# Kernel tuning notes

Measured on AMD Instinct MI355X. Metric: run time of the kernel, lower is better.

The kernel has to match this reference:

```python
import jax, jax.numpy as jnp
from jax import lax
import numpy as np

# ---- init hyperparameters (from init_kwargs) ----
STRIDE = 1
DP_CHANNELS = 1
ATOM_R = 8
ATOM_C = 8
NUMB_ATOM = 128
T_SC = 3
K = 256
BATCH = 32
IMG = 64


def setup_inputs() -> dict:
    key = jax.random.key(0)
    k1, k2 = jax.random.split(key)
    Y = jax.random.normal(k1, (BATCH, DP_CHANNELS, IMG, IMG), dtype=jnp.float32)
    # ConvTranspose2d weight layout: (numb_atom, dp_channels, atom_c, atom_r)
    W = jax.random.normal(k2, (NUMB_ATOM, DP_CHANNELS, ATOM_C, ATOM_R), dtype=jnp.float32)
    # normalise_weights(): each (i, j) filter divided by its L2 norm
    W = W / jnp.sqrt(jnp.sum(W ** 2, axis=(2, 3), keepdims=True))
    return {"Y": Y, "W_D": W}


def _conv_D(X, W):
    # PyTorch ConvTranspose2d (stride=1, no padding): full convolution with
    # spatially-flipped kernel; W is (in=numb_atom, out=dp_channels, kh, kw).
    kh, kw = W.shape[2], W.shape[3]
    return lax.conv_general_dilated(
        X, jnp.flip(W, (2, 3)), (1, 1),
        [(kh - 1, kh - 1), (kw - 1, kw - 1)],
        dimension_numbers=('NCHW', 'IOHW', 'NCHW'))


def _conv_Dt(R, Wt):
    # PyTorch Conv2d (VALID, stride=1): Wt is (out=numb_atom, in=dp, kh, kw)
    return lax.conv_general_dilated(
        R, Wt, (1, 1), 'VALID', dimension_numbers=('NCHW', 'OIHW', 'NCHW'))


def _hard_threshold_k(X, k):
    # keep the k largest-|.| entries per sample (over flattened C,H,W)
    B = X.shape[0]
    flat = X.reshape(B, -1)
    _, idx = lax.top_k(jnp.abs(flat), k)                      # [B, k]
    vals = jnp.take_along_axis(flat, idx, axis=1)             # [B, k]
    out = jnp.zeros_like(flat).at[jnp.arange(B)[:, None], idx].set(vals)
    return out.reshape(X.shape)


def _linesearch(Y, X, W, Wt, k):
    R = Y - _conv_D(X, W)
    g = _conv_Dt(R, Wt)
    l2_start = jnp.sum(R ** 2)

    def attempt(alpha):
        Xu = _hard_threshold_k(X + alpha * g, k)
        err = jnp.sum((Y - _conv_D(Xu, W)) ** 2)
        return Xu, err

    Xu0, err0 = attempt(jnp.float32(1.0))

    def cond(s):
        _, _, err, count = s
        return (err >= l2_start) & (count <= 15)

    def body(s):
        alpha, _, _, count = s
        alpha = alpha * jnp.float32(0.5)
        Xu, err = attempt(alpha)
        return (alpha, Xu, err, count + 1)

    alpha, Xu, err, _ = lax.while_loop(
        cond, body, (jnp.float32(1.0), Xu0, err0, jnp.int32(0)))
    return Xu, err, alpha


def reference(Y, W_D):
    # D_trans.weight = D.weight.permute(0,1,3,2) -> (numb_atom, dp, atom_r, atom_c)
    Wt = jnp.swapaxes(W_D, 2, 3)
    kh, kw = Wt.shape[2], Wt.shape[3]
    B, _, H, W_sp = Y.shape
    X = jnp.zeros((B, W_D.shape[0], H - kh + 1, W_sp - kw + 1), dtype=Y.dtype)
    for _ in range(T_SC):
        X, _, _ = _linesearch(Y, X, W_D, Wt, K)
    return X
```

## Files before the change

### kernel.cpp

```cpp
#include <hip/hip_runtime.h>
#include <stdint.h>

#define NB   32
#define NCH  128
#define IMG  64
#define IMG2 4096
#define OH   57
#define OHW  3249
#define CHW  415872
#define KTOP 256
#define NATT 17
#define NS   32
#define SCAP 512
#define NCAP 1536
#define NBUCK 8192
#define HSHIFT 18
#define TGT  512
#define RSTRIDE 72
#define NZB  257
#define BMW  12996

typedef unsigned long long ull;

__global__ void k_init(int* support_cnt) {
    if (threadIdx.x < NB) support_cnt[threadIdx.x] = 0;
}

__global__ __launch_bounds__(256) void k_resid(
    const float* __restrict__ Y, const float* __restrict__ W,
    const int* __restrict__ support_cnt, const uint32_t* __restrict__ support_idx,
    const float* __restrict__ support_val, float* __restrict__ Rg, double* __restrict__ l2part,
    uint32_t* __restrict__ hist, int* __restrict__ cand_cnt)
{
    int bx = blockIdx.x, tid = threadIdx.x;
    if (bx >= NB) {
        int zb = bx - NB;
        if (zb < 256) {
            ((uint4*)hist)[zb * 256 + tid] = make_uint4(0u, 0u, 0u, 0u);
        } else {
            ((uint4*)cand_cnt)[tid] = make_uint4(0u, 0u, 0u, 0u);
        }
        return;
    }
    int b = bx;
    __shared__ float Rs[IMG2];
    const float4* Y4 = (const float4*)(Y + b * IMG2);
    float4* R4 = (float4*)Rs;
    for (int i = tid; i < IMG2 / 4; i += 256) R4[i] = Y4[i];
    __syncthreads();
    int n = support_cnt[b];
    for (int task = tid; task < n * 64; task += 256) {
        int i = task >> 6, tap = task & 63, p = tap >> 3, q = tap & 7;
        uint32_t idx = support_idx[b * KTOP + i];
        float val = support_val[b * KTOP + i];
        int c = idx / OHW, rem = idx % OHW, s = rem / OH, t = rem % OH;
        float w = W[c * 64 + p * 8 + q];
        atomicAdd(&Rs[(s + p) * IMG + (t + q)], -val * w);
    }
    __syncthreads();
    double acc = 0.0;
    for (int i = tid; i < IMG2; i += 256) {
        float v = Rs[i];
        Rg[b * IMG2 + i] = v;
        acc += (double)v * (double)v;
    }
    __shared__ double red[256];
    red[tid] = acc; __syncthreads();
    for (int s2 = 128; s2 > 0; s2 >>= 1) { if (tid < s2) red[tid] += red[tid + s2]; __syncthreads(); }
    if (tid == 0) l2part[b] = red[0];
}

__global__ __launch_bounds__(256) void k_conv(
    const float* __restrict__ Rg, const float* __restrict__ W,
    float* __restrict__ g_out, uint32_t* __restrict__ hist)
{
    int b = blockIdx.x, cg0 = blockIdx.y, tid = threadIdx.x;
    __shared__ float Rs[71 * 72];
    __shared__ uint32_t hl[NBUCK];
    for (int i = tid; i < 71 * 72; i += 256) Rs[i] = 0.f;
    for (int i = tid; i < NBUCK; i += 256) hl[i] = 0u;
    __syncthreads();
    const float4* R4 = (const float4*)(Rg + b * IMG2);
    for (int i = tid; i < 1024; i += 256) {
        int row = i >> 4, col4 = (i & 15) * 4;
        *(float4*)&Rs[row * 72 + col4] = R4[i];
    }
    __syncthreads();
    int csub = tid >> 7;
    int tile = tid & 127;
    bool active = tile < 120;
    int tr = active ? tile / 15 : 0;
    int tc = active ? tile % 15 : 0;
    int s0 = tr * 8, t0 = tc * 4;

    for (int sub = 0; sub < 4; ++sub) {
        int c = cg0 * 8 + sub * 2 + csub;
        int c_s = __builtin_amdgcn_readfirstlane(c);
        const float* Wc = W + c_s * 64;

        float acc[8][4];
#pragma unroll
        for (int r = 0; r < 8; ++r)
#pragma unroll
            for (int cc = 0; cc < 4; ++cc) acc[r][cc] = 0.f;

#pragma unroll
        for (int rho = 0; rho < 15; ++rho) {
            float rb[12];
            const float* rp = &Rs[(s0 + rho) * 72 + t0];
            *(float4*)&rb[0] = *(const float4*)rp;
            *(float4*)&rb[4] = *(const float4*)(rp + 4);
            *(float4*)&rb[8] = *(const float4*)(rp + 8);
#pragma unroll
            for (int r = 0; r < 8; ++r) {
                const int p = rho - r;
                if (p >= 0 && p < 8) {
#pragma unroll
                    for (int q = 0; q < 8; ++q) {
                        float wv = Wc[q * 8 + p];
#pragma unroll
                        for (int cc = 0; cc < 4; ++cc)
                            acc[r][cc] = fmaf(rb[cc + q], wv, acc[r][cc]);
                    }
                }
            }
        }
        if (active) {
            float* go = g_out + (size_t)(b * NCH + c) * OHW;
#pragma unroll
            for (int r = 0; r < 8; ++r) {
                int s = s0 + r;
                if (s < OH) {
#pragma unroll
                    for (int cc = 0; cc < 4; ++cc) {
                        int t = t0 + cc;
                        if (t < OH) {
                            float v = acc[r][cc];
                            go[s * OH + t] = v;
                            uint32_t bits = __float_as_uint(v) & 0x7fffffffu;
                            atomicAdd(&hl[bits >> HSHIFT], 1u);
                        }
                    }
                }
            }
        }
    }
    __syncthreads();
    for (int i = tid; i < NBUCK; i += 256) {
        uint32_t v = hl[i];
        if (v) atomicAdd(&hist[b * NBUCK + i], v);
    }
}

__global__ __launch_bounds__(256) void k_thresh(const uint32_t* __restrict__ hist,
                                                uint32_t* __restrict__ thr) {
    int b = blockIdx.x, tid = threadIdx.x;
    uint32_t h[32];
    uint32_t s = 0;
    const uint32_t* hb = hist + b * NBUCK + tid * 32;
#pragma unroll
    for (int k = 0; k < 32; ++k) { h[k] = hb[k]; s += h[k]; }
    __shared__ uint32_t buf[2][256];
    int cur = 0;
    buf[0][tid] = s;
    __syncthreads();
    for (int d = 1; d < 256; d <<= 1) {
        uint32_t v = buf[cur][tid];
        if (tid + d < 256) v += buf[cur][tid + d];
        buf[cur ^ 1][tid] = v;
        cur ^= 1;
        __syncthreads();
    }
    uint32_t sufme = buf[cur][tid];
    uint32_t base  = (tid < 255) ? buf[cur][tid + 1] : 0u;
    if (tid == 0 && buf[cur][0] < TGT) thr[b] = 0u;
    if (base < TGT && sufme >= TGT) {
        uint32_t acc = base; int bk = 0;
#pragma unroll
        for (int k = 31; k >= 0; --k) {
            acc += h[k];
            if (acc >= TGT) { bk = tid * 32 + k; break; }
        }
        thr[b] = (uint32_t)bk << HSHIFT;
    }
}

__global__ __launch_bounds__(256) void k_collect(
    const float* __restrict__ g, const uint32_t* __restrict__ thr,
    int* __restrict__ cand_cnt, uint32_t* __restrict__ cand_idx, float* __restrict__ cand_g)
{
    int b = blockIdx.y;
    int i4 = blockIdx.x * 256 + threadIdx.x;
    if (i4 >= CHW / 4) return;
    int slice = blockIdx.x & (NS - 1);
    uint32_t tb = thr[b];
    float4 v4 = ((const float4*)(g + (size_t)b * CHW))[i4];
    float vv[4] = { v4.x, v4.y, v4.z, v4.w };
#pragma unroll
    for (int k = 0; k < 4; ++k) {
        uint32_t bits = __float_as_uint(vv[k]) & 0x7fffffffu;
        if (bits >= tb) {
            int pos = atomicAdd(&cand_cnt[b * NS + slice], 1);
            if (pos < SCAP) {
                cand_idx[(b * NS + slice) * SCAP + pos] = (uint32_t)(i4 * 4 + k);
                cand_g[(b * NS + slice) * SCAP + pos] = vv[k];
            }
        }
    }
}

__global__ __launch_bounds__(1024) void k_suppg(
    const float* __restrict__ g,
    const int* __restrict__ support_cnt, const uint32_t* __restrict__ support_idx,
    const int* __restrict__ cand_cnt, const uint32_t* __restrict__ cand_idx,
    const float* __restrict__ cand_g,
    uint32_t* __restrict__ ns_idx, float* __restrict__ ns_g, uint32_t* __restrict__ ns_pk,
    float* __restrict__ sup_g, uint32_t* __restrict__ sup_pk)
{
    int b = blockIdx.x, tid = threadIdx.x, lane = tid & 63;
    __shared__ uint32_t bm[BMW];
    __shared__ int cnts[NS];
    __shared__ ull ck[NCAP];
    __shared__ float cg_l[NCAP];
    __shared__ int nns_sh;
    int n = support_cnt[b];
    for (int i = tid; i < BMW / 4; i += 1024) ((uint4*)bm)[i] = make_uint4(0u, 0u, 0u, 0u);
    if (tid < NS) cnts[tid] = min(cand_cnt[b * NS + tid], SCAP);
    if (tid == 0) nns_sh = 0;
    __syncthreads();
    if (tid < KTOP) {
        if (tid < n) {
            uint32_t idx = support_idx[b * KTOP + tid];
            atomicOr(&bm[idx >> 5], 1u << (idx & 31));
            float gv = g[(size_t)b * CHW + idx];
            sup_g[b * KTOP + tid] = gv;
            int c = idx / OHW, r = idx % OHW, s = r / OH, t = r % OH;
            sup_pk[b * KTOP + tid] = (uint32_t)((c << 12) | (s << 6) | t);
        } else {
            sup_g[b * KTOP + tid] = 0.f;
            sup_pk[b * KTOP + tid] = 0u;
        }
    }
    __syncthreads();
    for (int t0 = tid; t0 < NS * SCAP; t0 += 1024) {
        int s = t0 >> 9, j = t0 & (SCAP - 1);
        bool keep = false; uint32_t idx = 0; float gv = 0.f;
        if (j < cnts[s]) {
            idx = cand_idx[(b * NS + s) * SCAP + j];
            gv = cand_g[(b * NS + s) * SCAP + j];
            keep = ((bm[idx >> 5] >> (idx & 31)) & 1u) == 0u;
        }
        ull mk = __ballot(keep);
        if (mk) {
            int basep = 0;
            if (lane == 0) basep = atomicAdd(&nns_sh, (int)__popcll(mk));
            basep = __shfl(basep, 0, 64);
            if (keep) {
                int p = basep + (int)__popcll(mk & ((1ull << lane) - 1ull));
                if (p < NCAP) {
                    ck[p] = ((ull)(__float_as_uint(gv) & 0x7fffffffu) << 32) | (ull)(uint32_t)(~idx);
                    cg_l[p] = gv;
                }
            }
        }
    }
    __syncthreads();
    int nns = min(nns_sh, NCAP);
    int nns8 = (nns + 7) & ~7;
    for (int i = nns + tid; i < nns8; i += 1024) ck[i] = 0ull;
    __syncthreads();
    ull myk[2]; int myr[2];
#pragma unroll
    for (int q = 0; q < 2; ++q) { int i = tid + 1024 * q; myk[q] = (i < nns) ? ck[i] : 0ull; myr[q] = 0; }
    for (int j = 0; j < nns8; j += 8) {
        ull t0 = ck[j], t1 = ck[j+1], t2 = ck[j+2], t3 = ck[j+3];
        ull t4 = ck[j+4], t5 = ck[j+5], t6 = ck[j+6], t7 = ck[j+7];
#pragma unroll
        for (int q = 0; q < 2; ++q) {
            myr[q] += ((t0 > myk[q]) ? 1 : 0) + ((t1 > myk[q]) ? 1 : 0)
                    + ((t2 > myk[q]) ? 1 : 0) + ((t3 > myk[q]) ? 1 : 0)
                    + ((t4 > myk[q]) ? 1 : 0) + ((t5 > myk[q]) ? 1 : 0)
                    + ((t6 > myk[q]) ? 1 : 0) + ((t7 > myk[q]) ? 1 : 0);
        }
    }
#pragma unroll
    for (int q = 0; q < 2; ++q) {
        int i = tid + 1024 * q;
        if (i < nns && myr[q] < KTOP) {
            uint32_t idx = ~(uint32_t)myk[q];
            int r = myr[q];
            ns_idx[b * KTOP + r] = idx;
            ns_g[b * KTOP + r] = cg_l[i];
            int c = idx / OHW, rr = idx % OHW, s = rr / OH, t = rr % OH;
            ns_pk[b * KTOP + r] = (uint32_t)((c << 12) | (s << 6) | t);
        }
    }
}

__global__ __launch_bounds__(1024) void k_att2(
    const float* __restrict__ Y, const float* __restrict__ W,
    const int* __restrict__ support_cnt, const uint32_t* __restrict__ support_idx,
    const float* __restrict__ support_val,
    const float* __restrict__ sup_g, const uint32_t* __restrict__ sup_pk,
    const uint32_t* __restrict__ ns_idx, const float* __restrict__ ns_g,
    const uint32_t* __restrict__ ns_pk,
    uint32_t* __restrict__ sel_idx, float* __restrict__ sel_val, double* __restrict__ err)
{
    int a = blockIdx.x, b = blockIdx.y, tid = threadIdx.x;
    int lane = tid & 63, wid = tid >> 6;
    float alpha = ldexpf(1.f, -a);
    int n = support_cnt[b];

    __shared__ float Wlds[NCH * 64];
    __shared__ float recon[64 * RSTRIDE];
    __shared__ ull kA[KTOP];
    __shared__ ull kB[KTOP];
    __shared__ float s_v[KTOP];
    __shared__ uint32_t s_pk2[KTOP];
    __shared__ double redd[16];

    uint32_t nsi = 0, pk_ns = 0, spi = 0, pk_sup = 0;
    float v_ns = 0.f, v_sup = 0.f;
    ull k_ns = 0, k_sup = 0;
    if (wid < 4) {
        nsi = ns_idx[b * KTOP + tid];
        v_ns = alpha * ns_g[b * KTOP + tid];
        pk_ns = ns_pk[b * KTOP + tid];
        k_ns = ((ull)(__float_as_uint(v_ns) & 0x7fffffffu) << 32) | (ull)(uint32_t)(~nsi);
        kA[tid] = k_ns;
        if (tid < n) {
            spi = support_idx[b * KTOP + tid];
            v_sup = fmaf(alpha, sup_g[b * KTOP + tid], support_val[b * KTOP + tid]);
            pk_sup = sup_pk[b * KTOP + tid];
        } else {
            spi = (uint32_t)(CHW + tid);
            v_sup = 0.f; pk_sup = 0u;
        }
        k_sup = ((ull)(__float_as_uint(v_sup) & 0x7fffffffu) << 32) | (ull)(uint32_t)(~spi);
        kB[tid] = k_sup;
    }
    __syncthreads();

    if (wid < 4) {
        int cb_ns = 0, cb_sup = 0;
        for (int j = 0; j < KTOP; j += 8) {
            ull t0 = kB[j], t1 = kB[j+1], t2 = kB[j+2], t3 = kB[j+3];
            ull t4 = kB[j+4], t5 = kB[j+5], t6 = kB[j+6], t7 = kB[j+7];
            cb_ns  += ((t0 > k_ns) ? 1 : 0) + ((t1 > k_ns) ? 1 : 0)
                    + ((t2 > k_ns) ? 1 : 0) + ((t3 > k_ns) ? 1 : 0)
                    + ((t4 > k_ns) ? 1 : 0) + ((t5 > k_ns) ? 1 : 0)
                    + ((t6 > k_ns) ? 1 : 0) + ((t7 > k_ns) ? 1 : 0);
            cb_sup += ((t0 > k_sup) ? 1 : 0) + ((t1 > k_sup) ? 1 : 0)
                    + ((t2 > k_sup) ? 1 : 0) + ((t3 > k_sup) ? 1 : 0)
                    + ((t4 > k_sup) ? 1 : 0) + ((t5 > k_sup) ? 1 : 0)
                    + ((t6 > k_sup) ? 1 : 0) + ((t7 > k_sup) ? 1 : 0);
        }
        int rank_ns = tid + cb_ns;
        int lo = 0, hi = KTOP;
        while (lo < hi) { int mid = (lo + hi) >> 1; if (kA[mid] > k_sup) lo = mid + 1; else hi = mid; }
        int rank_sup = lo + cb_sup;
        size_t o = ((size_t)a * NB + b) * KTOP;
        if (rank_ns < KTOP) {
            s_v[rank_ns] = v_ns; s_pk2[rank_ns] = pk_ns;
            sel_idx[o + rank_ns] = nsi; sel_val[o + rank_ns] = v_ns;
        }
        if (rank_sup < KTOP) {
            s_v[rank_sup] = v_sup; s_pk2[rank_sup] = pk_sup;
            sel_idx[o + rank_sup] = spi; sel_val[o + rank_sup] = v_sup;
        }
    } else {
        for (int i = tid - 256; i < 64 * RSTRIDE; i += 768) recon[i] = 0.f;
        for (int i = tid - 256; i < (NCH * 64) / 4; i += 768)
            ((float4*)Wlds)[i] = ((const float4*)W)[i];
    }
    __syncthreads();

    for (int task = tid; task < KTOP * 64; task += 1024) {
        int i = task >> 6, tap = task & 63, p = tap >> 3, q = tap & 7;
        uint32_t pk = s_pk2[i];
        float val = s_v[i];
        int c = pk >> 12, s = (pk >> 6) & 63, t = pk & 63;
        atomicAdd(&recon[(s + p) * RSTRIDE + (t + q)], val * Wlds[c * 64 + tap]);
    }
    __syncthreads();

    float4 y4 = ((const float4*)(Y + b * IMG2))[tid];
    int row = tid >> 4, col = (tid & 15) * 4;
    const float* rr = &recon[row * RSTRIDE + col];
    double accd = 0.0;
    float d0 = y4.x - rr[0]; accd += (double)d0 * (double)d0;
    float d1 = y4.y - rr[1]; accd += (double)d1 * (double)d1;
    float d2 = y4.z - rr[2]; accd += (double)d2 * (double)d2;
    float d3 = y4.w - rr[3]; accd += (double)d3 * (double)d3;
    for (int d = 32; d > 0; d >>= 1) accd += __shfl_xor(accd, d, 64);
    if (lane == 0) redd[wid] = accd;
    __syncthreads();
    if (tid == 0) {
        double e = 0.0;
#pragma unroll
        for (int w2 = 0; w2 < 16; ++w2) e += redd[w2];
        err[a * NB + b] = e;
    }
}

__global__ __launch_bounds__(256) void k_update(
    const double* __restrict__ l2part, const double* __restrict__ err,
    const uint32_t* __restrict__ sel_idx, const float* __restrict__ sel_val,
    int* __restrict__ support_cnt, uint32_t* __restrict__ support_idx, float* __restrict__ support_val)
{
    int b = blockIdx.x, tid = threadIdx.x;
    __shared__ double esum[NATT + 1];
    __shared__ int sel_sh;
    if (tid < NATT) {
        double e = 0.0;
        for (int b2 = 0; b2 < NB; ++b2) e += err[tid * NB + b2];
        esum[tid] = e;
    } else if (tid == NATT) {
        double l2 = 0.0;
        for (int b2 = 0; b2 < NB; ++b2) l2 += l2part[b2];
        esum[NATT] = l2;
    }
    __syncthreads();
    if (tid == 0) {
        double l2 = esum[NATT];
        int sel = NATT - 1;
        for (int a2 = 0; a2 < NATT; ++a2) if (esum[a2] < l2) { sel = a2; break; }
        sel_sh = sel;
    }
    __syncthreads();
    int a = sel_sh;
    __shared__ uint32_t ki[KTOP];
    __shared__ float kv[KTOP];
    ki[tid] = sel_idx[((size_t)a * NB + b) * KTOP + tid];
    kv[tid] = sel_val[((size_t)a * NB + b) * KTOP + tid];
    __syncthreads();
    uint32_t me = ki[tid];
    int rank = 0;
    for (int j = 0; j < KTOP; j += 8) {
        uint32_t a0 = ki[j], a1 = ki[j+1], a2 = ki[j+2], a3 = ki[j+3];
        uint32_t a4 = ki[j+4], a5 = ki[j+5], a6 = ki[j+6], a7 = ki[j+7];
        rank += ((a0 < me) ? 1 : 0) + ((a1 < me) ? 1 : 0) + ((a2 < me) ? 1 : 0) + ((a3 < me) ? 1 : 0)
              + ((a4 < me) ? 1 : 0) + ((a5 < me) ? 1 : 0) + ((a6 < me) ? 1 : 0) + ((a7 < me) ? 1 : 0);
    }
    support_idx[b * KTOP + rank] = me;
    support_val[b * KTOP + rank] = kv[tid];
    if (tid == 0) support_cnt[b] = KTOP;
}

__global__ void k_outzero(float4* __restrict__ out) {
    int i = blockIdx.x * 256 + threadIdx.x;
    if (i < (NB * CHW) / 4) out[i] = make_float4(0.f, 0.f, 0.f, 0.f);
}

__global__ void k_scatter(const uint32_t* __restrict__ support_idx, const float* __restrict__ support_val,
                          float* __restrict__ out) {
    int b = blockIdx.x, tid = threadIdx.x;
    if (tid < KTOP) out[(size_t)b * CHW + support_idx[b * KTOP + tid]] = support_val[b * KTOP + tid];
}

static size_t align256(size_t x) { return (x + 255) & ~(size_t)255; }

extern "C" void kernel_launch(void* const* d_in, const int* in_sizes, int n_in,
                              void* d_out, int out_size, void* d_ws, size_t ws_size,
                              hipStream_t stream)
{
    const float* Y = (const float*)d_in[0];
    const float* W = (const float*)d_in[1];
    float* out = (float*)d_out;

    char* p = (char*)d_ws;
    size_t off = 0;
    auto carve = [&](size_t bytes) { void* r = p + off; off = align256(off + bytes); return r; };
    float*    Rg          = (float*)   carve(NB * IMG2 * sizeof(float));
    uint32_t* hist        = (uint32_t*)carve((size_t)NB * NBUCK * sizeof(uint32_t));
    uint32_t* thr         = (uint32_t*)carve(NB * sizeof(uint32_t));
    int*      cand_cnt    = (int*)     carve(NB * NS * sizeof(int));
    double*   l2part      = (double*)  carve(NB * sizeof(double));
    double*   err         = (double*)  carve(NATT * NB * sizeof(double));
    int*      support_cnt = (int*)     carve(NB * sizeof(int));
    uint32_t* support_idx = (uint32_t*)carve(NB * KTOP * sizeof(uint32_t));
    float*    support_val = (float*)   carve(NB * KTOP * sizeof(float));
    uint32_t* sel_idx     = (uint32_t*)carve((size_t)NATT * NB * KTOP * sizeof(uint32_t));
    float*    sel_val     = (float*)   carve((size_t)NATT * NB * KTOP * sizeof(float));
    uint32_t* cand_idx    = (uint32_t*)carve((size_t)NB * NS * SCAP * sizeof(uint32_t));
    float*    cand_g      = (float*)   carve((size_t)NB * NS * SCAP * sizeof(float));
    uint32_t* ns_idx      = (uint32_t*)carve(NB * KTOP * sizeof(uint32_t));
    float*    ns_gbuf     = (float*)   carve(NB * KTOP * sizeof(float));
    uint32_t* ns_pk       = (uint32_t*)carve(NB * KTOP * sizeof(uint32_t));
    float*    sup_gbuf    = (float*)   carve(NB * KTOP * sizeof(float));
    uint32_t* sup_pk      = (uint32_t*)carve(NB * KTOP * sizeof(uint32_t));
    (void)ws_size; (void)in_sizes; (void)n_in; (void)out_size;

    k_init<<<1, 64, 0, stream>>>(support_cnt);
    for (int t = 0; t < 3; ++t) {
        k_resid<<<NB + NZB, 256, 0, stream>>>(Y, W, support_cnt, support_idx, support_val,
                                              Rg, l2part, hist, cand_cnt);
        k_conv<<<dim3(NB, 16), 256, 0, stream>>>(Rg, W, out, hist);
        k_thresh<<<NB, 256, 0, stream>>>(hist, thr);
        k_collect<<<dim3((CHW / 4 + 255) / 256, NB), 256, 0, stream>>>(out, thr, cand_cnt, cand_idx, cand_g);
        k_suppg<<<NB, 1024, 0, stream>>>(out, support_cnt, support_idx,
                                         cand_cnt, cand_idx, cand_g,
                                         ns_idx, ns_gbuf, ns_pk, sup_gbuf, sup_pk);
        k_att2<<<dim3(NATT, NB), 1024, 0, stream>>>(Y, W, support_cnt, support_idx, support_val,
                                                    sup_gbuf, sup_pk, ns_idx, ns_gbuf, ns_pk,
                                                    sel_idx, sel_val, err);
        k_update<<<NB, 256, 0, stream>>>(l2part, err, sel_idx, sel_val,
                                         support_cnt, support_idx, support_val);
    }
    k_outzero<<<((NB * CHW) / 4 + 255) / 256, 256, 0, stream>>>((float4*)out);
    k_scatter<<<NB, 256, 0, stream>>>(support_idx, support_val, out);
}
```

Baseline: 671.0 us.

## Fuse candidate selection and all line-search attempts into one per-sample kernel

Merges the support/candidate ranking kernel and the per-alpha attempt kernel into one 1024-thread block per sample. That block loops serially over all 17 step sizes, keeping Y, W and the candidate lists in shared memory. The support update is folded into the start of the residual kernel, and the final scatter reads the selected attempt directly. Together this removes the init, update and scatter launches and several global round-trips. The cost is parallelism: the attempt grid shrinks from 17×32 blocks to 32 blocks, so the 17 attempts now run one after another on few compute units.

```diff
diff --git a/kernel.cpp b/kernel.cpp
--- a/kernel.cpp
+++ b/kernel.cpp
@@ -22,14 +22,12 @@
 
 typedef unsigned long long ull;
 
-__global__ void k_init(int* support_cnt) {
-    if (threadIdx.x < NB) support_cnt[threadIdx.x] = 0;
-}
-
 __global__ __launch_bounds__(256) void k_resid(
     const float* __restrict__ Y, const float* __restrict__ W,
-    const int* __restrict__ support_cnt, const uint32_t* __restrict__ support_idx,
-    const float* __restrict__ support_val, float* __restrict__ Rg, double* __restrict__ l2part,
+    int do_update, const double* __restrict__ l2_prev, const double* __restrict__ errv,
+    const uint32_t* __restrict__ sel_idx, const float* __restrict__ sel_val,
+    uint32_t* __restrict__ support_idx, float* __restrict__ support_val,
+    float* __restrict__ Rg, double* __restrict__ l2_out,
     uint32_t* __restrict__ hist, int* __restrict__ cand_cnt)
 {
     int bx = blockIdx.x, tid = threadIdx.x;
@@ -43,16 +41,49 @@
         return;
     }
     int b = bx;
+    __shared__ uint32_t sidx_l[KTOP];
+    __shared__ float sval_l[KTOP];
+    __shared__ double esum[NATT + 1];
+    __shared__ int sel_sh;
+    int n = 0;
+    if (do_update) {
+        if (tid < NATT) {
+            double e = 0.0;
+            for (int b2 = 0; b2 < NB; ++b2) e += errv[tid * NB + b2];
+            esum[tid] = e;
+        } else if (tid == NATT) {
+            double l2 = 0.0;
+            for (int b2 = 0; b2 < NB; ++b2) l2 += l2_prev[b2];
+            esum[NATT] = l2;
+        }
+        __syncthreads();
+        if (tid == 0) {
+            double l2 = esum[NATT];
+            int sel = NATT - 1;
+            for (int a2 = 0; a2 < NATT; ++a2) if (esum[a2] < l2) { sel = a2; break; }
+            sel_sh = sel;
+        }
+        __syncthreads();
+        int a = sel_sh;
+        size_t o = ((size_t)a * NB + b) * KTOP + tid;
+        uint32_t ii = sel_idx[o];
+        float vv = sel_val[o];
+        sidx_l[tid] = ii; sval_l[tid] = vv;
+        support_idx[b * KTOP + tid] = ii;
+        support_val[b * KTOP + tid] = vv;
+        n = KTOP;
+    }
+    __syncthreads();
+
     __shared__ float Rs[IMG2];
     const float4* Y4 = (const float4*)(Y + b * IMG2);
     float4* R4 = (float4*)Rs;
     for (int i = tid; i < IMG2 / 4; i += 256) R4[i] = Y4[i];
     __syncthreads();
-    int n = support_cnt[b];
     for (int task = tid; task < n * 64; task += 256) {
         int i = task >> 6, tap = task & 63, p = tap >> 3, q = tap & 7;
-        uint32_t idx = support_idx[b * KTOP + i];
-        float val = support_val[b * KTOP + i];
+        uint32_t idx = sidx_l[i];
+        float val = sval_l[i];
         int c = idx / OHW, rem = idx % OHW, s = rem / OH, t = rem % OH;
         float w = W[c * 64 + p * 8 + q];
         atomicAdd(&Rs[(s + p) * IMG + (t + q)], -val * w);
@@ -67,7 +98,7 @@
     __shared__ double red[256];
     red[tid] = acc; __syncthreads();
     for (int s2 = 128; s2 > 0; s2 >>= 1) { if (tid < s2) red[tid] += red[tid + s2]; __syncthreads(); }
-    if (tid == 0) l2part[b] = red[0];
+    if (tid == 0) l2_out[b] = red[0];
 }
 
 __global__ __launch_bounds__(256) void k_conv(
@@ -209,36 +240,45 @@
     }
 }
 
-__global__ __launch_bounds__(1024) void k_suppg(
-    const float* __restrict__ g,
-    const int* __restrict__ support_cnt, const uint32_t* __restrict__ support_idx,
+__global__ __launch_bounds__(1024) void k_fat(
+    const float* __restrict__ g, const float* __restrict__ Y, const float* __restrict__ W,
+    int n_sup, const uint32_t* __restrict__ support_idx, const float* __restrict__ support_val,
     const int* __restrict__ cand_cnt, const uint32_t* __restrict__ cand_idx,
     const float* __restrict__ cand_g,
-    uint32_t* __restrict__ ns_idx, float* __restrict__ ns_g, uint32_t* __restrict__ ns_pk,
-    float* __restrict__ sup_g, uint32_t* __restrict__ sup_pk)
+    uint32_t* __restrict__ sel_idx, float* __restrict__ sel_val, double* __restrict__ err)
 {
-    int b = blockIdx.x, tid = threadIdx.x, lane = tid & 63;
-    __shared__ uint32_t bm[BMW];
-    __shared__ int cnts[NS];
+    int b = blockIdx.x, tid = threadIdx.x, lane = tid & 63, wid = tid >> 6;
+    __shared__ union UU {
+        uint32_t bm[BMW];
+        struct { float Y[IMG2]; float W[NCH * 64]; } yw;
+    } u;
     __shared__ ull ck[NCAP];
     __shared__ float cg_l[NCAP];
-    __shared__ int nns_sh;
-    int n = support_cnt[b];
-    for (int i = tid; i < BMW / 4; i += 1024) ((uint4*)bm)[i] = make_uint4(0u, 0u, 0u, 0u);
+    __shared__ float recon[64 * RSTRIDE];
+    __shared__ uint32_t A_idx[KTOP]; __shared__ float A_g[KTOP]; __shared__ uint32_t A_pk[KTOP];
+    __shared__ uint32_t B_idx[KTOP]; __shared__ float B_x[KTOP];
+    __shared__ float B_g[KTOP]; __shared__ uint32_t B_pk[KTOP];
+    __shared__ ull kA[KTOP]; __shared__ ull kB[KTOP];
+    __shared__ float s_v[KTOP]; __shared__ uint32_t s_pk2[KTOP];
+    __shared__ double redd[16];
+    __shared__ int cnts[NS]; __shared__ int nns_sh;
+
+    for (int i = tid; i < BMW / 4; i += 1024) ((uint4*)u.bm)[i] = make_uint4(0u, 0u, 0u, 0u);
     if (tid < NS) cnts[tid] = min(cand_cnt[b * NS + tid], SCAP);
     if (tid == 0) nns_sh = 0;
     __syncthreads();
     if (tid < KTOP) {
-        if (tid < n) {
+        if (tid < n_sup) {
             uint32_t idx = support_idx[b * KTOP + tid];
-            atomicOr(&bm[idx >> 5], 1u << (idx & 31));
-            float gv = g[(size_t)b * CHW + idx];
-            sup_g[b * KTOP + tid] = gv;
+            atomicOr(&u.bm[idx >> 5], 1u << (idx & 31));
+            B_idx[tid] = idx;
+            B_x[tid] = support_val[b * KTOP + tid];
+            B_g[tid] = g[(size_t)b * CHW + idx];
             int c = idx / OHW, r = idx % OHW, s = r / OH, t = r % OH;
-            sup_pk[b * KTOP + tid] = (uint32_t)((c << 12) | (s << 6) | t);
+            B_pk[tid] = (uint32_t)((c << 12) | (s << 6) | t);
         } else {
-            sup_g[b * KTOP + tid] = 0.f;
-            sup_pk[b * KTOP + tid] = 0u;
+            B_idx[tid] = (uint32_t)(CHW + tid);
+            B_x[tid] = 0.f; B_g[tid] = 0.f; B_pk[tid] = 0u;
         }
     }
     __syncthreads();
@@ -248,7 +288,7 @@
         if (j < cnts[s]) {
             idx = cand_idx[(b * NS + s) * SCAP + j];
             gv = cand_g[(b * NS + s) * SCAP + j];
-            keep = ((bm[idx >> 5] >> (idx & 31)) & 1u) == 0u;
+            keep = ((u.bm[idx >> 5] >> (idx & 31)) & 1u) == 0u;
         }
         ull mk = __ballot(keep);
         if (mk) {
@@ -256,10 +296,10 @@
             if (lane == 0) basep = atomicAdd(&nns_sh, (int)__popcll(mk));
             basep = __shfl(basep, 0, 64);
             if (keep) {
-                int p = basep + (int)__popcll(mk & ((1ull << lane) - 1ull));
-                if (p < NCAP) {
-                    ck[p] = ((ull)(__float_as_uint(gv) & 0x7fffffffu) << 32) | (ull)(uint32_t)(~idx);
-                    cg_l[p] = gv;
+                int p2 = basep + (int)__popcll(mk & ((1ull << lane) - 1ull));
+                if (p2 < NCAP) {
+                    ck[p2] = ((ull)(__float_as_uint(gv) & 0x7fffffffu) << 32) | (ull)(uint32_t)(~idx);
+                    cg_l[p2] = gv;
                 }
             }
         }
@@ -269,155 +309,144 @@
     int nns8 = (nns + 7) & ~7;
     for (int i = nns + tid; i < nns8; i += 1024) ck[i] = 0ull;
     __syncthreads();
-    ull myk[2]; int myr[2];
-#pragma unroll
-    for (int q = 0; q < 2; ++q) { int i = tid + 1024 * q; myk[q] = (i < nns) ? ck[i] : 0ull; myr[q] = 0; }
-    for (int j = 0; j < nns8; j += 8) {
-        ull t0 = ck[j], t1 = ck[j+1], t2 = ck[j+2], t3 = ck[j+3];
-        ull t4 = ck[j+4], t5 = ck[j+5], t6 = ck[j+6], t7 = ck[j+7];
+    {
+        ull myk[2]; int myr[2];
+#pragma unroll
+        for (int q = 0; q < 2; ++q) { int i = tid + 1024 * q; myk[q] = (i < nns) ? ck[i] : 0ull; myr[q] = 0; }
+        for (int j = 0; j < nns8; j += 8) {
+            ull t0 = ck[j], t1 = ck[j+1], t2 = ck[j+2], t3 = ck[j+3];
+            ull t4 = ck[j+4], t5 = ck[j+5], t6 = ck[j+6], t7 = ck[j+7];
+#pragma unroll
+            for (int q = 0; q < 2; ++q) {
+                myr[q] += ((t0 > myk[q]) ? 1 : 0) + ((t1 > myk[q]) ? 1 : 0)
+                        + ((t2 > myk[q]) ? 1 : 0) + ((t3 > myk[q]) ? 1 : 0)
+                        + ((t4 > myk[q]) ? 1 : 0) + ((t5 > myk[q]) ? 1 : 0)
+                        + ((t6 > myk[q]) ? 1 : 0) + ((t7 > myk[q]) ? 1 : 0);
+            }
+        }
 #pragma unroll
         for (int q = 0; q < 2; ++q) {
-            myr[q] += ((t0 > myk[q]) ? 1 : 0) + ((t1 > myk[q]) ? 1 : 0)
-                    + ((t2 > myk[q]) ? 1 : 0) + ((t3 > myk[q]) ? 1 : 0)
-                    + ((t4 > myk[q]) ? 1 : 0) + ((t5 > myk[q]) ? 1 : 0)
-                    + ((t6 > myk[q]) ? 1 : 0) + ((t7 > myk[q]) ? 1 : 0);
-        }
-    }
-#pragma unroll
-    for (int q = 0; q < 2; ++q) {
-        int i = tid + 1024 * q;
-        if (i < nns && myr[q] < KTOP) {
-            uint32_t idx = ~(uint32_t)myk[q];
-            int r = myr[q];
-            ns_idx[b * KTOP + r] = idx;
-            ns_g[b * KTOP + r] = cg_l[i];
-            int c = idx / OHW, rr = idx % OHW, s = rr / OH, t = rr % OH;
-            ns_pk[b * KTOP + r] = (uint32_t)((c << 12) | (s << 6) | t);
-        }
-    }
-}
-
-__global__ __launch_bounds__(1024) void k_att2(
-    const float* __restrict__ Y, const float* __restrict__ W,
-    const int* __restrict__ support_cnt, const uint32_t* __restrict__ support_idx,
-    const float* __restrict__ support_val,
-    const float* __restrict__ sup_g, const uint32_t* __restrict__ sup_pk,
-    const uint32_t* __restrict__ ns_idx, const float* __restrict__ ns_g,
-    const uint32_t* __restrict__ ns_pk,
-    uint32_t* __restrict__ sel_idx, float* __restrict__ sel_val, double* __restrict__ err)
-{
-    int a = blockIdx.x, b = blockIdx.y, tid = threadIdx.x;
-    int lane = tid & 63, wid = tid >> 6;
-    float alpha = ldexpf(1.f, -a);
-    int n = support_cnt[b];
-
-    __shared__ float Wlds[NCH * 64];
-    __shared__ float recon[64 * RSTRIDE];
-    __shared__ ull kA[KTOP];
-    __shared__ ull kB[KTOP];
-    __shared__ float s_v[KTOP];
-    __shared__ uint32_t s_pk2[KTOP];
-    __shared__ double redd[16];
-
-    uint32_t nsi = 0, pk_ns = 0, spi = 0, pk_sup = 0;
-    float v_ns = 0.f, v_sup = 0.f;
-    ull k_ns = 0, k_sup = 0;
-    if (wid < 4) {
-        nsi = ns_idx[b * KTOP + tid];
-        v_ns = alpha * ns_g[b * KTOP + tid];
-        pk_ns = ns_pk[b * KTOP + tid];
-        k_ns = ((ull)(__float_as_uint(v_ns) & 0x7fffffffu) << 32) | (ull)(uint32_t)(~nsi);
-        kA[tid] = k_ns;
-        if (tid < n) {
-            spi = support_idx[b * KTOP + tid];
-            v_sup = fmaf(alpha, sup_g[b * KTOP + tid], support_val[b * KTOP + tid]);
-            pk_sup = sup_pk[b * KTOP + tid];
+            int i = tid + 1024 * q;
+            if (i < nns && myr[q] < KTOP) {
+                uint32_t idx = ~(uint32_t)myk[q];
+                int r = myr[q];
+                A_idx[r] = idx;
+                A_g[r] = cg_l[i];
+                int c = idx / OHW, rr = idx % OHW, s = rr / OH, t = rr % OH;
+                A_pk[r] = (uint32_t)((c << 12) | (s << 6) | t);
+            }
+        }
+    }
+    for (int i = tid; i < IMG2 / 4; i += 1024)
+        ((float4*)u.yw.Y)[i] = ((const float4*)(Y + b * IMG2))[i];
+    for (int i = tid; i < (NCH * 64) / 4; i += 1024)
+        ((float4*)u.yw.W)[i] = ((const float4*)W)[i];
+    __syncthreads();
+
+    for (int a = 0; a < NATT; ++a) {
+        float alpha = ldexpf(1.f, -a);
+        float v_ns = 0.f, v_sup = 0.f;
+        ull k_ns = 0, k_sup = 0;
+        if (tid < KTOP) {
+            v_ns = alpha * A_g[tid];
+            k_ns = ((ull)(__float_as_uint(v_ns) & 0x7fffffffu) << 32) | (ull)(uint32_t)(~A_idx[tid]);
+            kA[tid] = k_ns;
+            v_sup = fmaf(alpha, B_g[tid], B_x[tid]);
+            k_sup = ((ull)(__float_as_uint(v_sup) & 0x7fffffffu) << 32) | (ull)(uint32_t)(~B_idx[tid]);
+            kB[tid] = k_sup;
         } else {
-            spi = (uint32_t)(CHW + tid);
-            v_sup = 0.f; pk_sup = 0u;
-        }
-        k_sup = ((ull)(__float_as_uint(v_sup) & 0x7fffffffu) << 32) | (ull)(uint32_t)(~spi);
-        kB[tid] = k_sup;
-    }
-    __syncthreads();
-
-    if (wid < 4) {
-        int cb_ns = 0, cb_sup = 0;
-        for (int j = 0; j < KTOP; j += 8) {
-            ull t0 = kB[j], t1 = kB[j+1], t2 = kB[j+2], t3 = kB[j+3];
-            ull t4 = kB[j+4], t5 = kB[j+5], t6 = kB[j+6], t7 = kB[j+7];
-            cb_ns  += ((t0 > k_ns) ? 1 : 0) + ((t1 > k_ns) ? 1 : 0)
-                    + ((t2 > k_ns) ? 1 : 0) + ((t3 > k_ns) ? 1 : 0)
-                    + ((t4 > k_ns) ? 1 : 0) + ((t5 > k_ns) ? 1 : 0)
-                    + ((t6 > k_ns) ? 1 : 0) + ((t7 > k_ns) ? 1 : 0);
-            cb_sup += ((t0 > k_sup) ? 1 : 0) + ((t1 > k_sup) ? 1 : 0)
-                    + ((t2 > k_sup) ? 1 : 0) + ((t3 > k_sup) ? 1 : 0)
-                    + ((t4 > k_sup) ? 1 : 0) + ((t5 > k_sup) ? 1 : 0)
-                    + ((t6 > k_sup) ? 1 : 0) + ((t7 > k_sup) ? 1 : 0);
-        }
-        int rank_ns = tid + cb_ns;
-        int lo = 0, hi = KTOP;
-        while (lo < hi) { int mid = (lo + hi) >> 1; if (kA[mid] > k_sup) lo = mid + 1; else hi = mid; }
-        int rank_sup = lo + cb_sup;
-        size_t o = ((size_t)a * NB + b) * KTOP;
-        if (rank_ns < KTOP) {
-            s_v[rank_ns] = v_ns; s_pk2[rank_ns] = pk_ns;
-            sel_idx[o + rank_ns] = nsi; sel_val[o + rank_ns] = v_ns;
-        }
-        if (rank_sup < KTOP) {
-            s_v[rank_sup] = v_sup; s_pk2[rank_sup] = pk_sup;
-            sel_idx[o + rank_sup] = spi; sel_val[o + rank_sup] = v_sup;
-        }
-    } else {
-        for (int i = tid - 256; i < 64 * RSTRIDE; i += 768) recon[i] = 0.f;
-        for (int i = tid - 256; i < (NCH * 64) / 4; i += 768)
-            ((float4*)Wlds)[i] = ((const float4*)W)[i];
-    }
-    __syncthreads();
-
-    for (int task = tid; task < KTOP * 64; task += 1024) {
-        int i = task >> 6, tap = task & 63, p = tap >> 3, q = tap & 7;
-        uint32_t pk = s_pk2[i];
-        float val = s_v[i];
-        int c = pk >> 12, s = (pk >> 6) & 63, t = pk & 63;
-        atomicAdd(&recon[(s + p) * RSTRIDE + (t + q)], val * Wlds[c * 64 + tap]);
-    }
-    __syncthreads();
-
-    float4 y4 = ((const float4*)(Y + b * IMG2))[tid];
-    int row = tid >> 4, col = (tid & 15) * 4;
-    const float* rr = &recon[row * RSTRIDE + col];
-    double accd = 0.0;
-    float d0 = y4.x - rr[0]; accd += (double)d0 * (double)d0;
-    float d1 = y4.y - rr[1]; accd += (double)d1 * (double)d1;
-    float d2 = y4.z - rr[2]; accd += (double)d2 * (double)d2;
-    float d3 = y4.w - rr[3]; accd += (double)d3 * (double)d3;
-    for (int d = 32; d > 0; d >>= 1) accd += __shfl_xor(accd, d, 64);
-    if (lane == 0) redd[wid] = accd;
-    __syncthreads();
-    if (tid == 0) {
-        double e = 0.0;
-#pragma unroll
-        for (int w2 = 0; w2 < 16; ++w2) e += redd[w2];
-        err[a * NB + b] = e;
-    }
-}
-
-__global__ __launch_bounds__(256) void k_update(
-    const double* __restrict__ l2part, const double* __restrict__ err,
+            for (int i = tid - 256; i < 64 * RSTRIDE; i += 768) recon[i] = 0.f;
+        }
+        __syncthreads();
+        if (tid < KTOP) {
+            int cb_ns = 0, cb_sup = 0;
+            for (int j = 0; j < KTOP; j += 8) {
+                ull t0 = kB[j], t1 = kB[j+1], t2 = kB[j+2], t3 = kB[j+3];
+                ull t4 = kB[j+4], t5 = kB[j+5], t6 = kB[j+6], t7 = kB[j+7];
+                cb_ns  += ((t0 > k_ns) ? 1 : 0) + ((t1 > k_ns) ? 1 : 0)
+                        + ((t2 > k_ns) ? 1 : 0) + ((t3 > k_ns) ? 1 : 0)
+                        + ((t4 > k_ns) ? 1 : 0) + ((t5 > k_ns) ? 1 : 0)
+                        + ((t6 > k_ns) ? 1 : 0) + ((t7 > k_ns) ? 1 : 0);
+                cb_sup += ((t0 > k_sup) ? 1 : 0) + ((t1 > k_sup) ? 1 : 0)
+                        + ((t2 > k_sup) ? 1 : 0) + ((t3 > k_sup) ? 1 : 0)
+                        + ((t4 > k_sup) ? 1 : 0) + ((t5 > k_sup) ? 1 : 0)
+                        + ((t6 > k_sup) ? 1 : 0) + ((t7 > k_sup) ? 1 : 0);
+            }
+            int rank_ns = tid + cb_ns;
+            int lo = 0, hi = KTOP;
+            while (lo < hi) { int mid = (lo + hi) >> 1; if (kA[mid] > k_sup) lo = mid + 1; else hi = mid; }
+            int rank_sup = lo + cb_sup;
+            size_t o = ((size_t)a * NB + b) * KTOP;
+            if (rank_ns < KTOP) {
+                s_v[rank_ns] = v_ns; s_pk2[rank_ns] = A_pk[tid];
+                sel_idx[o + rank_ns] = A_idx[tid]; sel_val[o + rank_ns] = v_ns;
+            }
+            if (rank_sup < KTOP) {
+                s_v[rank_sup] = v_sup; s_pk2[rank_sup] = B_pk[tid];
+                sel_idx[o + rank_sup] = B_idx[tid]; sel_val[o + rank_sup] = v_sup;
+            }
+        }
+        __syncthreads();
+        {
+            int tap = lane, p = tap >> 3, q = tap & 7;
+            uint32_t pks[16]; float vals[16];
+#pragma unroll
+            for (int it = 0; it < 16; ++it) {
+                int i = wid + it * 16;
+                pks[it] = s_pk2[i]; vals[it] = s_v[i];
+            }
+            float wv[16];
+#pragma unroll
+            for (int it = 0; it < 16; ++it) wv[it] = u.yw.W[(pks[it] >> 12) * 64 + tap];
+#pragma unroll
+            for (int it = 0; it < 16; ++it) {
+                uint32_t pk = pks[it];
+                int s = (pk >> 6) & 63, t = pk & 63;
+                atomicAdd(&recon[(s + p) * RSTRIDE + (t + q)], vals[it] * wv[it]);
+            }
+        }
+        __syncthreads();
+        float4 y4 = ((const float4*)u.yw.Y)[tid];
+        int row = tid >> 4, col = (tid & 15) * 4;
+        const float* rr = &recon[row * RSTRIDE + col];
+        double accd = 0.0;
+        float d0 = y4.x - rr[0]; accd += (double)d0 * (double)d0;
+        float d1 = y4.y - rr[1]; accd += (double)d1 * (double)d1;
+        float d2 = y4.z - rr[2]; accd += (double)d2 * (double)d2;
+        float d3 = y4.w - rr[3]; accd += (double)d3 * (double)d3;
+        for (int d = 32; d > 0; d >>= 1) accd += __shfl_xor(accd, d, 64);
+        if (lane == 0) redd[wid] = accd;
+        __syncthreads();
+        if (tid == 0) {
+            double e = 0.0;
+#pragma unroll
+            for (int w2 = 0; w2 < 16; ++w2) e += redd[w2];
+            err[a * NB + b] = e;
+        }
+        __syncthreads();
+    }
+}
+
+__global__ void k_outzero(float4* __restrict__ out) {
+    int i = blockIdx.x * 256 + threadIdx.x;
+    if (i < (NB * CHW) / 4) out[i] = make_float4(0.f, 0.f, 0.f, 0.f);
+}
+
+__global__ __launch_bounds__(256) void k_scafin(
+    const double* __restrict__ l2_prev, const double* __restrict__ errv,
     const uint32_t* __restrict__ sel_idx, const float* __restrict__ sel_val,
-    int* __restrict__ support_cnt, uint32_t* __restrict__ support_idx, float* __restrict__ support_val)
+    float* __restrict__ out)
 {
     int b = blockIdx.x, tid = threadIdx.x;
     __shared__ double esum[NATT + 1];
     __shared__ int sel_sh;
     if (tid < NATT) {
         double e = 0.0;
-        for (int b2 = 0; b2 < NB; ++b2) e += err[tid * NB + b2];
+        for (int b2 = 0; b2 < NB; ++b2) e += errv[tid * NB + b2];
         esum[tid] = e;
     } else if (tid == NATT) {
         double l2 = 0.0;
-        for (int b2 = 0; b2 < NB; ++b2) l2 += l2part[b2];
+        for (int b2 = 0; b2 < NB; ++b2) l2 += l2_prev[b2];
         esum[NATT] = l2;
     }
     __syncthreads();
@@ -429,33 +458,8 @@
     }
     __syncthreads();
     int a = sel_sh;
-    __shared__ uint32_t ki[KTOP];
-    __shared__ float kv[KTOP];
-    ki[tid] = sel_idx[((size_t)a * NB + b) * KTOP + tid];
-    kv[tid] = sel_val[((size_t)a * NB + b) * KTOP + tid];
-    __syncthreads();
-    uint32_t me = ki[tid];
-    int rank = 0;
-    for (int j = 0; j < KTOP; j += 8) {
-        uint32_t a0 = ki[j], a1 = ki[j+1], a2 = ki[j+2], a3 = ki[j+3];
-        uint32_t a4 = ki[j+4], a5 = ki[j+5], a6 = ki[j+6], a7 = ki[j+7];
-        rank += ((a0 < me) ? 1 : 0) + ((a1 < me) ? 1 : 0) + ((a2 < me) ? 1 : 0) + ((a3 < me) ? 1 : 0)
-              + ((a4 < me) ? 1 : 0) + ((a5 < me) ? 1 : 0) + ((a6 < me) ? 1 : 0) + ((a7 < me) ? 1 : 0);
-    }
-    support_idx[b * KTOP + rank] = me;
-    support_val[b * KTOP + rank] = kv[tid];
-    if (tid == 0) support_cnt[b] = KTOP;
-}
-
-__global__ void k_outzero(float4* __restrict__ out) {
-    int i = blockIdx.x * 256 + threadIdx.x;
-    if (i < (NB * CHW) / 4) out[i] = make_float4(0.f, 0.f, 0.f, 0.f);
-}
-
-__global__ void k_scatter(const uint32_t* __restrict__ support_idx, const float* __restrict__ support_val,
-                          float* __restrict__ out) {
-    int b = blockIdx.x, tid = threadIdx.x;
-    if (tid < KTOP) out[(size_t)b * CHW + support_idx[b * KTOP + tid]] = support_val[b * KTOP + tid];
+    size_t o = ((size_t)a * NB + b) * KTOP + tid;
+    out[(size_t)b * CHW + sel_idx[o]] = sel_val[o];
 }
 
 static size_t align256(size_t x) { return (x + 255) & ~(size_t)255; }
@@ -475,38 +479,28 @@
     uint32_t* hist        = (uint32_t*)carve((size_t)NB * NBUCK * sizeof(uint32_t));
     uint32_t* thr         = (uint32_t*)carve(NB * sizeof(uint32_t));
     int*      cand_cnt    = (int*)     carve(NB * NS * sizeof(int));
-    double*   l2part      = (double*)  carve(NB * sizeof(double));
+    double*   l2buf       = (double*)  carve(2 * NB * sizeof(double));
     double*   err         = (double*)  carve(NATT * NB * sizeof(double));
-    int*      support_cnt = (int*)     carve(NB * sizeof(int));
     uint32_t* support_idx = (uint32_t*)carve(NB * KTOP * sizeof(uint32_t));
     float*    support_val = (float*)   carve(NB * KTOP * sizeof(float));
     uint32_t* sel_idx     = (uint32_t*)carve((size_t)NATT * NB * KTOP * sizeof(uint32_t));
     float*    sel_val     = (float*)   carve((size_t)NATT * NB * KTOP * sizeof(float));
     uint32_t* cand_idx    = (uint32_t*)carve((size_t)NB * NS * SCAP * sizeof(uint32_t));
     float*    cand_g      = (float*)   carve((size_t)NB * NS * SCAP * sizeof(float));
-    uint32_t* ns_idx      = (uint32_t*)carve(NB * KTOP * sizeof(uint32_t));
-    float*    ns_gbuf     = (float*)   carve(NB * KTOP * sizeof(float));
-    uint32_t* ns_pk       = (uint32_t*)carve(NB * KTOP * sizeof(uint32_t));
-    float*    sup_gbuf    = (float*)   carve(NB * KTOP * sizeof(float));
-    uint32_t* sup_pk      = (uint32_t*)carve(NB * KTOP * sizeof(uint32_t));
     (void)ws_size; (void)in_sizes; (void)n_in; (void)out_size;
 
-    k_init<<<1, 64, 0, stream>>>(support_cnt);
     for (int t = 0; t < 3; ++t) {
-        k_resid<<<NB + NZB, 256, 0, stream>>>(Y, W, support_cnt, support_idx, support_val,
-                                              Rg, l2part, hist, cand_cnt);
+        double* l2_out  = l2buf + (t % 2) * NB;
+        double* l2_prev = l2buf + ((t + 1) % 2) * NB;
+        k_resid<<<NB + NZB, 256, 0, stream>>>(Y, W, (t > 0) ? 1 : 0, l2_prev, err,
+                                              sel_idx, sel_val, support_idx, support_val,
+                                              Rg, l2_out, hist, cand_cnt);
         k_conv<<<dim3(NB, 16), 256, 0, stream>>>(Rg, W, out, hist);
         k_thresh<<<NB, 256, 0, stream>>>(hist, thr);
         k_collect<<<dim3((CHW / 4 + 255) / 256, NB), 256, 0, stream>>>(out, thr, cand_cnt, cand_idx, cand_g);
-        k_suppg<<<NB, 1024, 0, stream>>>(out, support_cnt, support_idx,
-                                         cand_cnt, cand_idx, cand_g,
-                                         ns_idx, ns_gbuf, ns_pk, sup_gbuf, sup_pk);
-        k_att2<<<dim3(NATT, NB), 1024, 0, stream>>>(Y, W, support_cnt, support_idx, support_val,
-                                                    sup_gbuf, sup_pk, ns_idx, ns_gbuf, ns_pk,
-                                                    sel_idx, sel_val, err);
-        k_update<<<NB, 256, 0, stream>>>(l2part, err, sel_idx, sel_val,
-                                         support_cnt, support_idx, support_val);
+        k_fat<<<NB, 1024, 0, stream>>>(out, Y, W, (t > 0) ? KTOP : 0, support_idx, support_val,
+                                       cand_cnt, cand_idx, cand_g, sel_idx, sel_val, err);
     }
     k_outzero<<<((NB * CHW) / 4 + 255) / 256, 256, 0, stream>>>((float4*)out);
-    k_scatter<<<NB, 256, 0, stream>>>(support_idx, support_val, out);
-}
+    k_scafin<<<NB, 256, 0, stream>>>(l2buf + 0, err, sel_idx, sel_val, out);
+}
```

Result: slower. 1.807 ms (+169.3%).
